# Kernel tuning notes

Measured on AMD Instinct MI355X. Metric: run time of the kernel, lower is better.

## Reference

```python
import jax, jax.numpy as jnp
import numpy as np

N_HEADS = 8
OUT_FEATURES = 64
LEAKY_SLOPE = 0.2
MASK_FILL = -1e9


def setup_inputs() -> dict:
    key = jax.random.key(0)
    k_h, k_adj, k_W, k_a = jax.random.split(key, 4)
    B, N, F_IN = 1, 4096, 128
    h = jax.random.normal(k_h, (B, N, F_IN), dtype=jnp.float32)
    adj_mat = jax.random.randint(k_adj, (N, N), 0, 2, dtype=jnp.int32)
    # glorot-style scaled params
    W = jax.random.normal(k_W, (F_IN, OUT_FEATURES * N_HEADS), dtype=jnp.float32) * (1.0 / np.sqrt(F_IN))
    a = jax.random.normal(k_a, (N_HEADS, 2 * OUT_FEATURES, 1), dtype=jnp.float32) * (1.0 / np.sqrt(2 * OUT_FEATURES))
    return {"h": h, "adj_mat": adj_mat, "W": W, "a": a}


def reference(h, adj_mat, W, a):
    B, N, _ = h.shape
    heads = a.shape[0]
    out = a.shape[1] // 2
    # linear transform + head split (same reshape order as tf.reshape)
    ht = jnp.reshape(h @ W, (-1, heads, N, out))            # (B, heads, N, out)
    # additive attention scores
    src = jnp.einsum('bhnf,hfo->bhno', ht, a[:, :out, :])    # (B, heads, N, 1)
    tgt = jnp.einsum('bhnf,hfo->bhno', ht, a[:, out:, :])    # (B, heads, N, 1)
    e = src + jnp.swapaxes(tgt, -1, -2)                      # (B, heads, N, N)
    e = jnp.where(e > 0, e, LEAKY_SLOPE * e)                 # leaky_relu
    e = jnp.where(adj_mat > 0, e, MASK_FILL)                 # adjacency mask
    attention = jax.nn.softmax(e, axis=-1)
    h_prime = attention @ ht                                 # (B, heads, N, out)
    return h_prime
```

## Files before the change

kernel.cpp:

```cpp
#include <hip/hip_runtime.h>
#include <stdint.h>

#define HT_STRIDE 262144

typedef __attribute__((ext_vector_type(8))) short bf16x8;
typedef __attribute__((ext_vector_type(4))) float f32x4;

__device__ __forceinline__ unsigned short f2bf(float f) {
    unsigned int u = __float_as_uint(f);
    u += 0x7FFFu + ((u >> 16) & 1u);
    return (unsigned short)(u >> 16);
}

__global__ void __launch_bounds__(256) k_linear(const float* __restrict__ h,
                                                const float* __restrict__ W,
                                                float* __restrict__ ht) {
    __shared__ float hs[8][128];
    const int t = threadIdx.x;
    const int n0 = blockIdx.x * 8;
    {
        float4 v = ((const float4*)(h + n0 * 128))[t];
        int e = t * 4;
        int r = e >> 7, f = e & 127;
        hs[r][f + 0] = v.x; hs[r][f + 1] = v.y;
        hs[r][f + 2] = v.z; hs[r][f + 3] = v.w;
    }
    __syncthreads();
    float acc0[8], acc1[8];
    #pragma unroll
    for (int r = 0; r < 8; ++r) { acc0[r] = 0.f; acc1[r] = 0.f; }
    const float2* Wf = (const float2*)W;
    for (int f = 0; f < 128; ++f) {
        float2 wp = Wf[f * 256 + t];
        #pragma unroll
        for (int r = 0; r < 8; ++r) {
            float hv = hs[r][f];
            acc0[r] = fmaf(hv, wp.x, acc0[r]);
            acc1[r] = fmaf(hv, wp.y, acc1[r]);
        }
    }
    float2* ob = (float2*)ht;
    #pragma unroll
    for (int r = 0; r < 8; ++r) {
        ob[(n0 + r) * 256 + t] = make_float2(acc0[r], acc1[r]);
    }
}

__global__ void __launch_bounds__(256) k_prep(const float* __restrict__ ht,
                                              const float* __restrict__ aW,
                                              float* __restrict__ src,
                                              float* __restrict__ tgt,
                                              unsigned short* __restrict__ htT2) {
    __shared__ float ldsA[64][65];
    __shared__ float redS[4][64];
    __shared__ float redT[4][64];
    const int t = threadIdx.x;
    const int p0 = blockIdx.x * 64;
    const int hd = p0 >> 12;
    const int m0 = p0 & 4095;

    {
        const float4* g = (const float4*)(ht + p0 * 64);
        #pragma unroll
        for (int i = 0; i < 4; ++i) {
            int fid = t + 256 * i;
            float4 v = g[fid];
            int r = fid >> 4, o4 = (fid & 15) * 4;
            ldsA[r][o4 + 0] = v.x; ldsA[r][o4 + 1] = v.y;
            ldsA[r][o4 + 2] = v.z; ldsA[r][o4 + 3] = v.w;
        }
    }
    __syncthreads();

    {
        const int r = t & 63, og = t >> 6;
        float s = 0.f, g2 = 0.f;
        #pragma unroll
        for (int k = 0; k < 16; ++k) {
            int o = og * 16 + k;
            float hv = ldsA[r][o];
            s  = fmaf(hv, aW[hd * 128 + o], s);
            g2 = fmaf(hv, aW[hd * 128 + 64 + o], g2);
        }
        redS[og][r] = s; redT[og][r] = g2;
    }
    __syncthreads();
    if (t < 64) {
        src[p0 + t] = redS[0][t] + redS[1][t] + redS[2][t] + redS[3][t];
    } else if (t < 128) {
        int r = t - 64;
        tgt[p0 + r] = redT[0][r] + redT[1][r] + redT[2][r] + redT[3][r];
    }

    unsigned short* d = htT2 + (hd * 128 + (m0 >> 5)) * 2048;
    #pragma unroll
    for (int i = 0; i < 16; ++i) {
        int id = t + 256 * i;
        int mi = id & 31, o = (id >> 5) & 63, ct = id >> 11;
        d[ct * 2048 + o * 32 + mi] = f2bf(ldsA[mi + 32 * ct][o]);
    }
}

__global__ void __launch_bounds__(256) k_adjmask(const int* __restrict__ adj,
                                                 unsigned int* __restrict__ abm) {
    __shared__ unsigned int ldsT[1024];
    const int t = threadIdx.x;
    const int lane = t & 63;
    const int w = t >> 6;
    const int s = blockIdx.x >> 3;
    const int cq = blockIdx.x & 7;
    for (int rr = 0; rr < 16; ++rr) {
        const int* arow = adj + (s * 64 + w * 16 + rr) * 4096 + cq * 512;
        int v[8];
        #pragma unroll
        for (int j = 0; j < 8; ++j) v[j] = arow[j * 64 + lane];
        #pragma unroll
        for (int j = 0; j < 8; ++j) {
            unsigned long long m = __ballot(v[j] > 0);
            if (lane < 2)
                ldsT[(2 * j + lane) * 64 + rr * 4 + w] = (unsigned int)(m >> (lane * 32));
        }
    }
    __syncthreads();
    ((uint4*)(abm + (s * 128 + cq * 16) * 64))[t] = ((uint4*)ldsT)[t];
}

__global__ void __launch_bounds__(256, 2) k_attn(const unsigned int* __restrict__ abm,
                                                 const unsigned short* __restrict__ htT2,
                                                 const float* __restrict__ srcv,
                                                 const float* __restrict__ tgtv,
                                                 float* __restrict__ out) {
    __shared__ __align__(16) float smem[13056];
    unsigned int* bm = (unsigned int*)smem;

    const int t = threadIdx.x;
    const int kq = t >> 6;
    const int lane = t & 63;
    const int li = lane & 15;
    const int quad = lane >> 4;
    const int head = blockIdx.x & 7;
    const int stripe = blockIdx.x >> 3;
    const int i0 = stripe * 64;

    {
        const uint4* gsrc = (const uint4*)(abm + stripe * 8192);
        uint4* dst = (uint4*)bm;
        #pragma unroll
        for (int i = 0; i < 8; ++i) dst[t + 256 * i] = gsrc[t + 256 * i];
    }

    float a_[4], b_[4];
    #pragma unroll
    for (int g = 0; g < 4; ++g) {
        float sv = srcv[head * 4096 + i0 + 16 * g + li];
        a_[g] = sv;
        b_[g] = 0.2f * sv;
    }

    f32x4 acc[16];
    #pragma unroll
    for (int i = 0; i < 16; ++i) acc[i] = (f32x4){0.f, 0.f, 0.f, 0.f};
    float pd[4] = {0.f, 0.f, 0.f, 0.f};

    const float4* tgtp = (const float4*)(tgtv + head * 4096);
    const uint4*  ap   = (const uint4*)(htT2 + head * HT_STRIDE) + (li * 4 + quad);

    __syncthreads();

    const int c0 = kq * 32;
    uint4 bw = ((const uint4*)bm)[c0 * 16 + li];
    float4 tg0 = tgtp[c0 * 8 + quad * 2 + 0];
    float4 tg1 = tgtp[c0 * 8 + quad * 2 + 1];
    uint4 av0 = ap[c0 * 256 + 0];
    uint4 av1 = ap[c0 * 256 + 64];
    uint4 av2 = ap[c0 * 256 + 128];
    uint4 av3 = ap[c0 * 256 + 192];

    #pragma unroll 1
    for (int ci = 0; ci < 32; ++ci) {
        const int cn = c0 + ((ci + 1) & 31);
        uint4 nbw = ((const uint4*)bm)[cn * 16 + li];
        float4 ntg0 = tgtp[cn * 8 + quad * 2 + 0];
        float4 ntg1 = tgtp[cn * 8 + quad * 2 + 1];
        uint4 nav0 = ap[cn * 256 + 0];
        uint4 nav1 = ap[cn * 256 + 64];
        uint4 nav2 = ap[cn * 256 + 128];
        uint4 nav3 = ap[cn * 256 + 192];

        const float tt[8] = {tg0.x, tg0.y, tg0.z, tg0.w, tg1.x, tg1.y, tg1.z, tg1.w};
        const unsigned int wb[4] = {bw.x, bw.y, bw.z, bw.w};
        #pragma unroll
        for (int g = 0; g < 4; ++g) {
            const unsigned int wq = wb[g] >> (quad * 8);
            float wv[8];
            #pragma unroll
            for (int j = 0; j < 8; ++j) {
                float t1 = tt[j] + a_[g];
                float t2 = fmaf(tt[j], 0.2f, b_[g]);
                float e = fmaxf(t1, t2);
                float p = __expf(e);
                wv[j] = (wq & (1u << j)) ? p : 0.f;
                pd[g] += wv[j];
            }
            unsigned int pk0, pk1, pk2, pk3;
            asm("v_cvt_pk_bf16_f32 %0, %1, %2" : "=v"(pk0) : "v"(wv[0]), "v"(wv[1]));
            asm("v_cvt_pk_bf16_f32 %0, %1, %2" : "=v"(pk1) : "v"(wv[2]), "v"(wv[3]));
            asm("v_cvt_pk_bf16_f32 %0, %1, %2" : "=v"(pk2) : "v"(wv[4]), "v"(wv[5]));
            asm("v_cvt_pk_bf16_f32 %0, %1, %2" : "=v"(pk3) : "v"(wv[6]), "v"(wv[7]));
            uint4 bv; bv.x = pk0; bv.y = pk1; bv.z = pk2; bv.w = pk3;
            bf16x8 bfrag = __builtin_bit_cast(bf16x8, bv);
            acc[g * 4 + 0] = __builtin_amdgcn_mfma_f32_16x16x32_bf16(__builtin_bit_cast(bf16x8, av0), bfrag, acc[g * 4 + 0], 0, 0, 0);
            acc[g * 4 + 1] = __builtin_amdgcn_mfma_f32_16x16x32_bf16(__builtin_bit_cast(bf16x8, av1), bfrag, acc[g * 4 + 1], 0, 0, 0);
            acc[g * 4 + 2] = __builtin_amdgcn_mfma_f32_16x16x32_bf16(__builtin_bit_cast(bf16x8, av2), bfrag, acc[g * 4 + 2], 0, 0, 0);
            acc[g * 4 + 3] = __builtin_amdgcn_mfma_f32_16x16x32_bf16(__builtin_bit_cast(bf16x8, av3), bfrag, acc[g * 4 + 3], 0, 0, 0);
        }
        bw = nbw; tg0 = ntg0; tg1 = ntg1;
        av0 = nav0; av1 = nav1; av2 = nav2; av3 = nav3;
    }

    __syncthreads();
    float* comb = smem;
    if (kq != 0) {
        float* cb = comb + ((kq - 1) * 64 + lane) * 68;
        #pragma unroll
        for (int i = 0; i < 16; ++i) ((f32x4*)cb)[i] = acc[i];
        #pragma unroll
        for (int g = 0; g < 4; ++g) cb[64 + g] = pd[g];
    }
    __syncthreads();
    if (kq == 0) {
        #pragma unroll
        for (int q = 0; q < 3; ++q) {
            const float* cb = comb + (q * 64 + lane) * 68;
            #pragma unroll
            for (int i = 0; i < 16; ++i) acc[i] += ((const f32x4*)cb)[i];
            #pragma unroll
            for (int g = 0; g < 4; ++g) pd[g] += cb[64 + g];
        }
        #pragma unroll
        for (int g = 0; g < 4; ++g) {
            float p2 = pd[g];
            p2 += __shfl_xor(p2, 16, 64);
            p2 += __shfl_xor(p2, 32, 64);
            const float rd = 1.0f / p2;
            float4* op = (float4*)(out + head * HT_STRIDE + (i0 + 16 * g + li) * 64);
            #pragma unroll
            for (int f = 0; f < 4; ++f) {
                f32x4 a = acc[g * 4 + f];
                op[f * 4 + quad] = make_float4(a[0] * rd, a[1] * rd, a[2] * rd, a[3] * rd);
            }
        }
    }
}

extern "C" void kernel_launch(void* const* d_in, const int* in_sizes, int n_in,
                              void* d_out, int out_size, void* d_ws, size_t ws_size,
                              hipStream_t stream) {
    const float* h   = (const float*)d_in[0];
    const int*   adj = (const int*)d_in[1];
    const float* W   = (const float*)d_in[2];
    const float* aW  = (const float*)d_in[3];
    float* out = (float*)d_out;

    char* ws = (char*)d_ws;
    float* src  = (float*)(ws);
    float* tgt  = (float*)(ws + 131072);
    unsigned int*   abm  = (unsigned int*)(ws + 262144);
    unsigned short* htT2 = (unsigned short*)(ws + 2359296);
    float* ht = out;

    hipLaunchKernelGGL(k_linear,  dim3(512), dim3(256), 0, stream, h, W, ht);
    hipLaunchKernelGGL(k_prep,    dim3(512), dim3(256), 0, stream, ht, aW, src, tgt, htT2);
    hipLaunchKernelGGL(k_adjmask, dim3(512), dim3(256), 0, stream, adj, abm);
    hipLaunchKernelGGL(k_attn,    dim3(512), dim3(256), 0, stream, abm, htT2, src, tgt, out);
}
```

Measured before the change: 177.1 us.

## Fuse prep kernels into one launch and halve attention row tiles for occupancy

Merges the linear transform, score/transposition prep, and adjacency bitmask kernels into one launch. Blocks are split by index between mask building and linear+prep, and the ht intermediate now stays in LDS instead of round-tripping through global memory. The attention kernel moves from 64-row to 32-row stripes with 1024 blocks, launch bounds of 4 blocks per CU, and less LDS. Its explicit register prefetch is dropped, and src/tgt are pre-scaled by log2(e) so the hardware exp2 can be used. The risk is lower per-block reuse of the htT2 loads and losing the software prefetch that hid load latency.

Result: faster. 156.8 us (-11.4%).

```diff
diff --git a/kernel.cpp b/kernel.cpp
--- a/kernel.cpp
+++ b/kernel.cpp
@@ -2,6 +2,7 @@
 #include <stdint.h>
 
 #define HT_STRIDE 262144
+#define LOG2E 1.4426950408889634f
 
 typedef __attribute__((ext_vector_type(8))) short bf16x8;
 typedef __attribute__((ext_vector_type(4))) float f32x4;
@@ -12,126 +13,124 @@
     return (unsigned short)(u >> 16);
 }
 
-__global__ void __launch_bounds__(256) k_linear(const float* __restrict__ h,
-                                                const float* __restrict__ W,
-                                                float* __restrict__ ht) {
+__device__ __forceinline__ float exp2_fast(float e) {
+#if __has_builtin(__builtin_amdgcn_exp2f)
+    return __builtin_amdgcn_exp2f(e);
+#else
+    return __expf(e * 0.6931471805599453f);
+#endif
+}
+
+__global__ void __launch_bounds__(256) k_fused(const float* __restrict__ h,
+                                               const int* __restrict__ adj,
+                                               const float* __restrict__ W,
+                                               const float* __restrict__ aW,
+                                               float* __restrict__ src,
+                                               float* __restrict__ tgt,
+                                               unsigned short* __restrict__ htT2,
+                                               unsigned int* __restrict__ abm) {
+    __shared__ unsigned int ldsT[1024];
     __shared__ float hs[8][128];
-    const int t = threadIdx.x;
-    const int n0 = blockIdx.x * 8;
-    {
-        float4 v = ((const float4*)(h + n0 * 128))[t];
-        int e = t * 4;
-        int r = e >> 7, f = e & 127;
-        hs[r][f + 0] = v.x; hs[r][f + 1] = v.y;
-        hs[r][f + 2] = v.z; hs[r][f + 3] = v.w;
-    }
-    __syncthreads();
-    float acc0[8], acc1[8];
-    #pragma unroll
-    for (int r = 0; r < 8; ++r) { acc0[r] = 0.f; acc1[r] = 0.f; }
-    const float2* Wf = (const float2*)W;
-    for (int f = 0; f < 128; ++f) {
-        float2 wp = Wf[f * 256 + t];
-        #pragma unroll
-        for (int r = 0; r < 8; ++r) {
-            float hv = hs[r][f];
-            acc0[r] = fmaf(hv, wp.x, acc0[r]);
-            acc1[r] = fmaf(hv, wp.y, acc1[r]);
-        }
-    }
-    float2* ob = (float2*)ht;
-    #pragma unroll
-    for (int r = 0; r < 8; ++r) {
-        ob[(n0 + r) * 256 + t] = make_float2(acc0[r], acc1[r]);
-    }
-}
-
-__global__ void __launch_bounds__(256) k_prep(const float* __restrict__ ht,
-                                              const float* __restrict__ aW,
-                                              float* __restrict__ src,
-                                              float* __restrict__ tgt,
-                                              unsigned short* __restrict__ htT2) {
-    __shared__ float ldsA[64][65];
+    __shared__ float ldsA[64][66];
     __shared__ float redS[4][64];
     __shared__ float redT[4][64];
     const int t = threadIdx.x;
-    const int p0 = blockIdx.x * 64;
-    const int hd = p0 >> 12;
-    const int m0 = p0 & 4095;
-
-    {
-        const float4* g = (const float4*)(ht + p0 * 64);
-        #pragma unroll
-        for (int i = 0; i < 4; ++i) {
-            int fid = t + 256 * i;
-            float4 v = g[fid];
-            int r = fid >> 4, o4 = (fid & 15) * 4;
-            ldsA[r][o4 + 0] = v.x; ldsA[r][o4 + 1] = v.y;
-            ldsA[r][o4 + 2] = v.z; ldsA[r][o4 + 3] = v.w;
-        }
-    }
-    __syncthreads();
-
-    {
-        const int r = t & 63, og = t >> 6;
-        float s = 0.f, g2 = 0.f;
-        #pragma unroll
-        for (int k = 0; k < 16; ++k) {
-            int o = og * 16 + k;
-            float hv = ldsA[r][o];
-            s  = fmaf(hv, aW[hd * 128 + o], s);
-            g2 = fmaf(hv, aW[hd * 128 + 64 + o], g2);
-        }
-        redS[og][r] = s; redT[og][r] = g2;
-    }
-    __syncthreads();
-    if (t < 64) {
-        src[p0 + t] = redS[0][t] + redS[1][t] + redS[2][t] + redS[3][t];
-    } else if (t < 128) {
-        int r = t - 64;
-        tgt[p0 + r] = redT[0][r] + redT[1][r] + redT[2][r] + redT[3][r];
-    }
-
-    unsigned short* d = htT2 + (hd * 128 + (m0 >> 5)) * 2048;
-    #pragma unroll
-    for (int i = 0; i < 16; ++i) {
-        int id = t + 256 * i;
-        int mi = id & 31, o = (id >> 5) & 63, ct = id >> 11;
-        d[ct * 2048 + o * 32 + mi] = f2bf(ldsA[mi + 32 * ct][o]);
-    }
-}
-
-__global__ void __launch_bounds__(256) k_adjmask(const int* __restrict__ adj,
-                                                 unsigned int* __restrict__ abm) {
-    __shared__ unsigned int ldsT[1024];
-    const int t = threadIdx.x;
-    const int lane = t & 63;
-    const int w = t >> 6;
-    const int s = blockIdx.x >> 3;
-    const int cq = blockIdx.x & 7;
-    for (int rr = 0; rr < 16; ++rr) {
-        const int* arow = adj + (s * 64 + w * 16 + rr) * 4096 + cq * 512;
-        int v[8];
-        #pragma unroll
-        for (int j = 0; j < 8; ++j) v[j] = arow[j * 64 + lane];
-        #pragma unroll
-        for (int j = 0; j < 8; ++j) {
-            unsigned long long m = __ballot(v[j] > 0);
-            if (lane < 2)
-                ldsT[(2 * j + lane) * 64 + rr * 4 + w] = (unsigned int)(m >> (lane * 32));
-        }
-    }
-    __syncthreads();
-    ((uint4*)(abm + (s * 128 + cq * 16) * 64))[t] = ((uint4*)ldsT)[t];
-}
-
-__global__ void __launch_bounds__(256, 2) k_attn(const unsigned int* __restrict__ abm,
+
+    if (blockIdx.x < 512) {
+        const int lane = t & 63;
+        const int w = t >> 6;
+        const int sb = blockIdx.x >> 3;
+        const int cq = blockIdx.x & 7;
+        for (int rr = 0; rr < 16; ++rr) {
+            const int* arow = adj + (sb * 64 + w * 16 + rr) * 4096 + cq * 512;
+            int v[8];
+            #pragma unroll
+            for (int j = 0; j < 8; ++j) v[j] = arow[j * 64 + lane];
+            #pragma unroll
+            for (int j = 0; j < 8; ++j) {
+                unsigned long long m = __ballot(v[j] > 0);
+                if (lane < 2)
+                    ldsT[(2 * j + lane) * 64 + rr * 4 + w] = (unsigned int)(m >> (lane * 32));
+            }
+        }
+        __syncthreads();
+        ((uint4*)(abm + (sb * 128 + cq * 16) * 64))[t] = ((uint4*)ldsT)[t];
+    } else {
+        const int bid2 = (int)blockIdx.x - 512;
+        const int n0 = bid2 * 8;
+        const int p0 = bid2 * 64;
+        const int hd = p0 >> 12;
+        const int m0 = p0 & 4095;
+
+        {
+            float4 v = ((const float4*)(h + n0 * 128))[t];
+            int e = t * 4;
+            int r = e >> 7, f = e & 127;
+            hs[r][f + 0] = v.x; hs[r][f + 1] = v.y;
+            hs[r][f + 2] = v.z; hs[r][f + 3] = v.w;
+        }
+        __syncthreads();
+
+        float acc0[8], acc1[8];
+        #pragma unroll
+        for (int r = 0; r < 8; ++r) { acc0[r] = 0.f; acc1[r] = 0.f; }
+        const float2* Wf = (const float2*)W;
+        for (int f = 0; f < 128; ++f) {
+            float2 wp = Wf[f * 256 + t];
+            #pragma unroll
+            for (int r = 0; r < 8; ++r) {
+                float hv = hs[r][f];
+                acc0[r] = fmaf(hv, wp.x, acc0[r]);
+                acc1[r] = fmaf(hv, wp.y, acc1[r]);
+            }
+        }
+        {
+            const int ns = t >> 5;
+            const int o = (2 * t) & 63;
+            #pragma unroll
+            for (int r = 0; r < 8; ++r) {
+                *(float2*)&ldsA[r * 8 + ns][o] = make_float2(acc0[r], acc1[r]);
+            }
+        }
+        __syncthreads();
+
+        {
+            const int r = t & 63, og = t >> 6;
+            float sdot = 0.f, gdot = 0.f;
+            #pragma unroll
+            for (int k = 0; k < 16; ++k) {
+                int o = og * 16 + k;
+                float hv = ldsA[r][o];
+                sdot = fmaf(hv, aW[hd * 128 + o], sdot);
+                gdot = fmaf(hv, aW[hd * 128 + 64 + o], gdot);
+            }
+            redS[og][r] = sdot; redT[og][r] = gdot;
+        }
+        __syncthreads();
+        if (t < 64) {
+            src[p0 + t] = (redS[0][t] + redS[1][t] + redS[2][t] + redS[3][t]) * LOG2E;
+        } else if (t < 128) {
+            int r = t - 64;
+            tgt[p0 + r] = (redT[0][r] + redT[1][r] + redT[2][r] + redT[3][r]) * LOG2E;
+        }
+
+        unsigned short* d = htT2 + (hd * 128 + (m0 >> 5)) * 2048;
+        #pragma unroll
+        for (int i = 0; i < 16; ++i) {
+            int id = t + 256 * i;
+            int mi = id & 31, o = (id >> 5) & 63, ct = id >> 11;
+            d[ct * 2048 + o * 32 + mi] = f2bf(ldsA[mi + 32 * ct][o]);
+        }
+    }
+}
+
+__global__ void __launch_bounds__(256, 4) k_attn(const unsigned int* __restrict__ abm,
                                                  const unsigned short* __restrict__ htT2,
                                                  const float* __restrict__ srcv,
                                                  const float* __restrict__ tgtv,
                                                  float* __restrict__ out) {
-    __shared__ __align__(16) float smem[13056];
-    unsigned int* bm = (unsigned int*)smem;
+    __shared__ __align__(16) float smem[6912];
+    uint2* bm2 = (uint2*)smem;
 
     const int t = threadIdx.x;
     const int kq = t >> 6;
@@ -139,28 +138,32 @@
     const int li = lane & 15;
     const int quad = lane >> 4;
     const int head = blockIdx.x & 7;
-    const int stripe = blockIdx.x >> 3;
-    const int i0 = stripe * 64;
+    const int s32 = blockIdx.x >> 3;
+    const int s64 = s32 >> 1, half = s32 & 1;
+    const int i0 = s32 * 32;
 
     {
-        const uint4* gsrc = (const uint4*)(abm + stripe * 8192);
-        uint4* dst = (uint4*)bm;
-        #pragma unroll
-        for (int i = 0; i < 8; ++i) dst[t + 256 * i] = gsrc[t + 256 * i];
-    }
-
-    float a_[4], b_[4];
+        const unsigned int* base = abm + s64 * 8192 + half * 2;
+        #pragma unroll
+        for (int i = 0; i < 8; ++i) {
+            int p = t + 256 * i;
+            int c = p >> 4, lw = p & 15;
+            bm2[p] = *(const uint2*)(base + c * 64 + lw * 4);
+        }
+    }
+
+    float a_[2], b_[2];
     #pragma unroll
-    for (int g = 0; g < 4; ++g) {
-        float sv = srcv[head * 4096 + i0 + 16 * g + li];
-        a_[g] = sv;
-        b_[g] = 0.2f * sv;
-    }
-
-    f32x4 acc[16];
+    for (int g2 = 0; g2 < 2; ++g2) {
+        float sv = srcv[head * 4096 + i0 + 16 * g2 + li];
+        a_[g2] = sv;
+        b_[g2] = 0.2f * sv;
+    }
+
+    f32x4 acc[8];
     #pragma unroll
-    for (int i = 0; i < 16; ++i) acc[i] = (f32x4){0.f, 0.f, 0.f, 0.f};
-    float pd[4] = {0.f, 0.f, 0.f, 0.f};
+    for (int i = 0; i < 8; ++i) acc[i] = (f32x4){0.f, 0.f, 0.f, 0.f};
+    float pd[2] = {0.f, 0.f};
 
     const float4* tgtp = (const float4*)(tgtv + head * 4096);
     const uint4*  ap   = (const uint4*)(htT2 + head * HT_STRIDE) + (li * 4 + quad);
@@ -168,39 +171,31 @@
     __syncthreads();
 
     const int c0 = kq * 32;
-    uint4 bw = ((const uint4*)bm)[c0 * 16 + li];
-    float4 tg0 = tgtp[c0 * 8 + quad * 2 + 0];
-    float4 tg1 = tgtp[c0 * 8 + quad * 2 + 1];
-    uint4 av0 = ap[c0 * 256 + 0];
-    uint4 av1 = ap[c0 * 256 + 64];
-    uint4 av2 = ap[c0 * 256 + 128];
-    uint4 av3 = ap[c0 * 256 + 192];
-
     #pragma unroll 1
     for (int ci = 0; ci < 32; ++ci) {
-        const int cn = c0 + ((ci + 1) & 31);
-        uint4 nbw = ((const uint4*)bm)[cn * 16 + li];
-        float4 ntg0 = tgtp[cn * 8 + quad * 2 + 0];
-        float4 ntg1 = tgtp[cn * 8 + quad * 2 + 1];
-        uint4 nav0 = ap[cn * 256 + 0];
-        uint4 nav1 = ap[cn * 256 + 64];
-        uint4 nav2 = ap[cn * 256 + 128];
-        uint4 nav3 = ap[cn * 256 + 192];
+        const int c = c0 + ci;
+        uint4 av0 = ap[c * 256 + 0];
+        uint4 av1 = ap[c * 256 + 64];
+        uint4 av2 = ap[c * 256 + 128];
+        uint4 av3 = ap[c * 256 + 192];
+        float4 tg0 = tgtp[c * 8 + quad * 2 + 0];
+        float4 tg1 = tgtp[c * 8 + quad * 2 + 1];
+        uint2 bw = bm2[c * 16 + li];
 
         const float tt[8] = {tg0.x, tg0.y, tg0.z, tg0.w, tg1.x, tg1.y, tg1.z, tg1.w};
-        const unsigned int wb[4] = {bw.x, bw.y, bw.z, bw.w};
-        #pragma unroll
-        for (int g = 0; g < 4; ++g) {
-            const unsigned int wq = wb[g] >> (quad * 8);
+        const unsigned int wb[2] = {bw.x, bw.y};
+        #pragma unroll
+        for (int g2 = 0; g2 < 2; ++g2) {
+            const unsigned int wq = wb[g2] >> (quad * 8);
             float wv[8];
             #pragma unroll
             for (int j = 0; j < 8; ++j) {
-                float t1 = tt[j] + a_[g];
-                float t2 = fmaf(tt[j], 0.2f, b_[g]);
+                float t1 = tt[j] + a_[g2];
+                float t2 = fmaf(tt[j], 0.2f, b_[g2]);
                 float e = fmaxf(t1, t2);
-                float p = __expf(e);
+                float p = exp2_fast(e);
                 wv[j] = (wq & (1u << j)) ? p : 0.f;
-                pd[g] += wv[j];
+                pd[g2] += wv[j];
             }
             unsigned int pk0, pk1, pk2, pk3;
             asm("v_cvt_pk_bf16_f32 %0, %1, %2" : "=v"(pk0) : "v"(wv[0]), "v"(wv[1]));
@@ -209,44 +204,39 @@
             asm("v_cvt_pk_bf16_f32 %0, %1, %2" : "=v"(pk3) : "v"(wv[6]), "v"(wv[7]));
             uint4 bv; bv.x = pk0; bv.y = pk1; bv.z = pk2; bv.w = pk3;
             bf16x8 bfrag = __builtin_bit_cast(bf16x8, bv);
-            acc[g * 4 + 0] = __builtin_amdgcn_mfma_f32_16x16x32_bf16(__builtin_bit_cast(bf16x8, av0), bfrag, acc[g * 4 + 0], 0, 0, 0);
-            acc[g * 4 + 1] = __builtin_amdgcn_mfma_f32_16x16x32_bf16(__builtin_bit_cast(bf16x8, av1), bfrag, acc[g * 4 + 1], 0, 0, 0);
-            acc[g * 4 + 2] = __builtin_amdgcn_mfma_f32_16x16x32_bf16(__builtin_bit_cast(bf16x8, av2), bfrag, acc[g * 4 + 2], 0, 0, 0);
-            acc[g * 4 + 3] = __builtin_amdgcn_mfma_f32_16x16x32_bf16(__builtin_bit_cast(bf16x8, av3), bfrag, acc[g * 4 + 3], 0, 0, 0);
-        }
-        bw = nbw; tg0 = ntg0; tg1 = ntg1;
-        av0 = nav0; av1 = nav1; av2 = nav2; av3 = nav3;
+            acc[g2 * 4 + 0] = __builtin_amdgcn_mfma_f32_16x16x32_bf16(__builtin_bit_cast(bf16x8, av0), bfrag, acc[g2 * 4 + 0], 0, 0, 0);
+            acc[g2 * 4 + 1] = __builtin_amdgcn_mfma_f32_16x16x32_bf16(__builtin_bit_cast(bf16x8, av1), bfrag, acc[g2 * 4 + 1], 0, 0, 0);
+            acc[g2 * 4 + 2] = __builtin_amdgcn_mfma_f32_16x16x32_bf16(__builtin_bit_cast(bf16x8, av2), bfrag, acc[g2 * 4 + 2], 0, 0, 0);
+            acc[g2 * 4 + 3] = __builtin_amdgcn_mfma_f32_16x16x32_bf16(__builtin_bit_cast(bf16x8, av3), bfrag, acc[g2 * 4 + 3], 0, 0, 0);
+        }
     }
 
     __syncthreads();
-    float* comb = smem;
     if (kq != 0) {
-        float* cb = comb + ((kq - 1) * 64 + lane) * 68;
-        #pragma unroll
-        for (int i = 0; i < 16; ++i) ((f32x4*)cb)[i] = acc[i];
-        #pragma unroll
-        for (int g = 0; g < 4; ++g) cb[64 + g] = pd[g];
+        float* cb = smem + ((kq - 1) * 64 + lane) * 36;
+        #pragma unroll
+        for (int i = 0; i < 8; ++i) ((f32x4*)cb)[i] = acc[i];
+        cb[32] = pd[0]; cb[33] = pd[1];
     }
     __syncthreads();
     if (kq == 0) {
         #pragma unroll
         for (int q = 0; q < 3; ++q) {
-            const float* cb = comb + (q * 64 + lane) * 68;
-            #pragma unroll
-            for (int i = 0; i < 16; ++i) acc[i] += ((const f32x4*)cb)[i];
-            #pragma unroll
-            for (int g = 0; g < 4; ++g) pd[g] += cb[64 + g];
-        }
-        #pragma unroll
-        for (int g = 0; g < 4; ++g) {
-            float p2 = pd[g];
+            const float* cb = smem + (q * 64 + lane) * 36;
+            #pragma unroll
+            for (int i = 0; i < 8; ++i) acc[i] += ((const f32x4*)cb)[i];
+            pd[0] += cb[32]; pd[1] += cb[33];
+        }
+        #pragma unroll
+        for (int g2 = 0; g2 < 2; ++g2) {
+            float p2 = pd[g2];
             p2 += __shfl_xor(p2, 16, 64);
             p2 += __shfl_xor(p2, 32, 64);
             const float rd = 1.0f / p2;
-            float4* op = (float4*)(out + head * HT_STRIDE + (i0 + 16 * g + li) * 64);
+            float4* op = (float4*)(out + head * HT_STRIDE + (i0 + 16 * g2 + li) * 64);
             #pragma unroll
             for (int f = 0; f < 4; ++f) {
-                f32x4 a = acc[g * 4 + f];
+                f32x4 a = acc[g2 * 4 + f];
                 op[f * 4 + quad] = make_float4(a[0] * rd, a[1] * rd, a[2] * rd, a[3] * rd);
             }
         }
@@ -267,10 +257,9 @@
     float* tgt  = (float*)(ws + 131072);
     unsigned int*   abm  = (unsigned int*)(ws + 262144);
     unsigned short* htT2 = (unsigned short*)(ws + 2359296);
-    float* ht = out;
-
-    hipLaunchKernelGGL(k_linear,  dim3(512), dim3(256), 0, stream, h, W, ht);
-    hipLaunchKernelGGL(k_prep,    dim3(512), dim3(256), 0, stream, ht, aW, src, tgt, htT2);
-    hipLaunchKernelGGL(k_adjmask, dim3(512), dim3(256), 0, stream, adj, abm);
-    hipLaunchKernelGGL(k_attn,    dim3(512), dim3(256), 0, stream, abm, htT2, src, tgt, out);
-}
+
+    hipLaunchKernelGGL(k_fused, dim3(1024), dim3(256), 0, stream,
+                       h, adj, W, aW, src, tgt, htT2, abm);
+    hipLaunchKernelGGL(k_attn,  dim3(1024), dim3(256), 0, stream,
+                       abm, htT2, src, tgt, out);
+}
```
